# Performance work log

Hardware: AMD Instinct MI355X
Metric: run time of the kernel (lower is better)

## Reference

```python
import jax, jax.numpy as jnp
import numpy as np

NUM_GRAPHS = 100
NODES_PER_GRAPH = 500
EDGES_PER_GRAPH = 4000
HIDDEN = 128
RATIO = 0.5


def setup_inputs() -> dict:
    key = jax.random.key(0)
    k1, k2, k3, k4, k5 = jax.random.split(key, 5)
    N = NUM_GRAPHS * NODES_PER_GRAPH
    E = NUM_GRAPHS * EDGES_PER_GRAPH
    emb = jax.random.normal(k1, (N, HIDDEN), dtype=jnp.float32)
    # edges stay within their own graph's node range
    offs = (jnp.arange(NUM_GRAPHS, dtype=jnp.int32) * NODES_PER_GRAPH)[:, None]
    src = jax.random.randint(k2, (NUM_GRAPHS, EDGES_PER_GRAPH), 0, NODES_PER_GRAPH, dtype=jnp.int32) + offs
    dst = jax.random.randint(k3, (NUM_GRAPHS, EDGES_PER_GRAPH), 0, NODES_PER_GRAPH, dtype=jnp.int32) + offs
    edge_index = jnp.stack([src.reshape(-1), dst.reshape(-1)], axis=0)  # [2, E]
    node_batch = jnp.repeat(jnp.arange(NUM_GRAPHS, dtype=jnp.int32), NODES_PER_GRAPH)  # [N]
    s1 = 1.0 / np.sqrt(2 * HIDDEN)
    s2 = 1.0 / np.sqrt(4 * HIDDEN)
    W1 = jax.random.normal(k4, (2 * HIDDEN, 4 * HIDDEN), dtype=jnp.float32) * s1
    b1 = jnp.zeros((4 * HIDDEN,), dtype=jnp.float32)
    W2 = jax.random.normal(k5, (4 * HIDDEN, 1), dtype=jnp.float32) * s2
    b2 = jnp.zeros((1,), dtype=jnp.float32)
    return {"emb": emb, "edge_index": edge_index, "node_batch": node_batch,
            "W1": W1, "b1": b1, "W2": W2, "b2": b2}


def reference(emb, edge_index, node_batch, W1, b1, W2, b2):
    row, col = edge_index[0], edge_index[1]
    E = row.shape[0]
    N = emb.shape[0]

    # --- edge attention: gather endpoint embeddings, concat, 2-layer MLP ---
    edge_rep = jnp.concatenate([emb[row], emb[col]], axis=-1)       # [E, 2H]
    h = jax.nn.relu(edge_rep @ W1 + b1)                              # [E, 4H]
    edge_att = (h @ W2 + b2)[:, 0]                                   # [E]

    # --- per-graph top-k split (split_graph with ratio) ---
    edge_graph = node_batch[row]                                     # [E]
    order = jnp.lexsort((-edge_att, edge_graph))                     # sort by graph, desc score
    counts = jax.ops.segment_sum(jnp.ones(E, jnp.int32), edge_graph,
                                 num_segments=NUM_GRAPHS)            # edges per graph
    offsets = jnp.concatenate([jnp.zeros(1, jnp.int32),
                               jnp.cumsum(counts)[:-1].astype(jnp.int32)])
    g_sorted = edge_graph[order]
    rank = jnp.arange(E, dtype=jnp.int32) - offsets[g_sorted]        # rank within graph
    k_per_graph = jnp.ceil(RATIO * counts.astype(jnp.float32)).astype(jnp.int32)
    causal_sorted = rank < k_per_graph[g_sorted]
    causal_mask = jnp.zeros(E, dtype=bool).at[order].set(causal_sorted)

    causal_edge_weight = jnp.where(causal_mask, edge_att, 0.0)
    spu_edge_weight = jnp.where(causal_mask, 0.0, edge_att)

    # --- relabel: compact node ids for the causal subgraph ---
    cm = causal_mask.astype(jnp.int32)
    deg = jnp.zeros(N, jnp.int32).at[row].add(cm).at[col].add(cm)
    node_mask = deg > 0                                              # nodes kept in causal subgraph
    new_id = jnp.cumsum(node_mask.astype(jnp.int32)) - 1             # compacted ids
    new_row = jnp.where(causal_mask, new_id[row], -1)
    new_col = jnp.where(causal_mask, new_id[col], -1)
    causal_edge_index = jnp.stack([new_row, new_col], axis=0)        # [2, E], -1 = dropped
    causal_x = jnp.where(node_mask[:, None], emb, 0.0)               # masked node features

    return (edge_att, causal_edge_weight, spu_edge_weight,
            causal_mask, causal_edge_index, node_mask, causal_x)
```

## Files before the change

kernel.cpp:

```cpp
#include <hip/hip_runtime.h>
#include <hip/hip_bf16.h>

#define NG      100
#define NPG     500
#define EPG     4000
#define HID     128
#define NNODES  (NG*NPG)
#define NE      (NG*EPG)
#define KSEL    2000
#define NB_SCAN ((NNODES + 255) / 256)

#define MAXB    1024
#define NRC     8
#define RJT     8
#define DELTA   0.03125f

#define O_ATT   0
#define O_CEW   (NE)
#define O_SEW   (2*NE)
#define O_MASK  (3*NE)
#define O_CEI   (4*NE)
#define O_NMASK (6*NE)
#define O_CX    (6*NE + NNODES)

typedef __attribute__((ext_vector_type(8))) short  short8;
typedef __attribute__((ext_vector_type(8))) __bf16 bf16x8;
typedef __attribute__((ext_vector_type(4))) float  f32x4;

#define MFMA16(a,b,c) __builtin_amdgcn_mfma_f32_16x16x32_bf16( \
    __builtin_bit_cast(bf16x8,(a)), __builtin_bit_cast(bf16x8,(b)), (c), 0, 0, 0)

#define GLOAD_LDS16(g, l) __builtin_amdgcn_global_load_lds( \
    (const __attribute__((address_space(1))) unsigned int*)(g), \
    (__attribute__((address_space(3)))       unsigned int*)(l), 16, 0, 0)

__device__ __forceinline__ unsigned short tobf(float x) {
    __hip_bfloat16 hb = __float2bfloat16(x);
    return *(unsigned short*)&hb;
}

#define PREP_TOBF 6250
#define PREP_PACK 512
#define PREP_DEG  49
#define PREP_GRID (PREP_TOBF + PREP_PACK + PREP_DEG + 1)

__global__ __launch_bounds__(256)
void prep_kernel(const float* __restrict__ emb, const float* __restrict__ W1,
                 unsigned short* __restrict__ eb, unsigned short* __restrict__ ph,
                 float* __restrict__ deg, int* __restrict__ bcnt)
{
    const int blk = blockIdx.x;
    const int t   = threadIdx.x;
    if (blk < PREP_TOBF) {
        int i = blk * 256 + t;
        float4 v = ((const float4*)emb)[i];
        ushort4 h;
        h.x = tobf(v.x); h.y = tobf(v.y); h.z = tobf(v.z); h.w = tobf(v.w);
        ((ushort4*)eb)[i] = h;
    } else if (blk < PREP_TOBF + PREP_PACK) {
        int idx  = (blk - PREP_TOBF) * 256 + t;
        int i    = idx & 7;
        int lane = (idx >> 3) & 63;
        int g    = idx >> 9;
        int jsub = g & 3;
        int rem  = g >> 2;
        int jo   = rem & 7;
        int kc   = rem >> 3;
        int j = jo * 64 + jsub * 16 + (lane & 15);
        int k = kc * 32 + (lane >> 4) * 8 + i;
        ph[idx] = tobf(W1[k * 512 + j]);
    } else if (blk < PREP_TOBF + PREP_PACK + PREP_DEG) {
        int i4 = (blk - PREP_TOBF - PREP_PACK) * 256 + t;
        if (i4 < NNODES / 4) ((float4*)deg)[i4] = make_float4(0.f, 0.f, 0.f, 0.f);
    } else {
        if (t < NG) bcnt[t] = 0;
    }
}

__global__ __launch_bounds__(256)
void att5_kernel(const unsigned short* __restrict__ embb,
                 const unsigned short* __restrict__ w1p,
                 const int* __restrict__ ei,
                 const float* __restrict__ b1,
                 const float* __restrict__ W2,
                 const float* __restrict__ b2,
                 float* __restrict__ out)
{
    __shared__ __align__(16) unsigned short ldsB[16384];

    const int t    = threadIdx.x;
    const int w    = t >> 6;
    const int lane = t & 63;
    const int r16  = lane & 15;
    const int quad = lane >> 4;

    const int e_base = blockIdx.x * 256 + w * 64;
    const char* eb = (const char*)embb;

    f32x4 A[4][8];
#pragma unroll
    for (int mt = 0; mt < 4; ++mt) {
        int e = min(e_base + mt * 16 + r16, NE - 1);
        const char* sp = eb + (ei[e] << 8);
        const char* dp = eb + (ei[NE + e] << 8);
#pragma unroll
        for (int k4 = 0; k4 < 4; ++k4) {
            A[mt][k4]     = *(const f32x4*)(sp + k4 * 64 + quad * 16);
            A[mt][k4 + 4] = *(const f32x4*)(dp + k4 * 64 + quad * 16);
        }
    }

    float attP[4][4];
#pragma unroll
    for (int mt = 0; mt < 4; ++mt)
#pragma unroll
        for (int rg = 0; rg < 4; ++rg) attP[mt][rg] = 0.0f;

#define STAGE(s_, buf_)                                                      \
    {                                                                        \
        _Pragma("unroll")                                                    \
        for (int cc = 0; cc < 4; ++cc) {                                     \
            int c2   = w * 4 + cc;                                           \
            int kc   = c2 >> 1;                                              \
            int jsub = ((s_) & 1) * 2 + (c2 & 1);                            \
            int jo   = (s_) >> 1;                                            \
            int g    = (kc * 8 + jo) * 4 + jsub;                             \
            GLOAD_LDS16(w1p + g * 512 + lane * 8,                            \
                        ldsB + (buf_) * 8192 + c2 * 512);                    \
        }                                                                    \
    }

    STAGE(0, 0);
    __syncthreads();

    for (int s = 0; s < 16; ++s) {
        const int cur = s & 1;
        if (s < 15) STAGE(s + 1, cur ^ 1);

#pragma unroll
        for (int jsub2 = 0; jsub2 < 2; ++jsub2) {
            f32x4 acc[4];
#pragma unroll
            for (int mt = 0; mt < 4; ++mt) acc[mt] = f32x4{};

#pragma unroll
            for (int kc = 0; kc < 8; ++kc) {
                short8 B = *(const short8*)(ldsB + cur * 8192 +
                                            (kc * 2 + jsub2) * 512 + lane * 8);
#pragma unroll
                for (int mt = 0; mt < 4; ++mt)
                    acc[mt] = MFMA16(A[mt][kc], B, acc[mt]);
            }

            const int j = s * 32 + jsub2 * 16 + r16;
            const float b1v = b1[j], w2v = W2[j];
#pragma unroll
            for (int mt = 0; mt < 4; ++mt)
#pragma unroll
                for (int rg = 0; rg < 4; ++rg)
                    attP[mt][rg] += fmaxf(acc[mt][rg] + b1v, 0.0f) * w2v;
        }
        __syncthreads();
    }
#undef STAGE

#pragma unroll
    for (int mt = 0; mt < 4; ++mt)
#pragma unroll
        for (int rg = 0; rg < 4; ++rg) {
            float v = attP[mt][rg];
#pragma unroll
            for (int msk = 1; msk <= 8; msk <<= 1) v += __shfl_xor(v, msk, 64);
            attP[mt][rg] = v;
        }

    const float bias2 = b2[0];
    if (r16 < 4) {
#pragma unroll
        for (int mt = 0; mt < 4; ++mt) {
            const int row = quad * 4 + r16;
            const int e   = e_base + mt * 16 + row;
            if (e < NE) out[O_ATT + e] = attP[mt][r16] + bias2;
        }
    }
}

__device__ __forceinline__ unsigned enc_key(float f) {
    unsigned u = __float_as_uint(f);
    return (u & 0x80000000u) ? ~u : (u | 0x80000000u);
}
__device__ __forceinline__ float dec_key(unsigned k) {
    unsigned u = (k & 0x80000000u) ? (k ^ 0x80000000u) : ~k;
    return __uint_as_float(u);
}

__device__ __forceinline__ int wave_sum(int c) {
#pragma unroll
    for (int m = 1; m <= 32; m <<= 1) c += __shfl_xor(c, m, 64);
    return c;
}

__global__ __launch_bounds__(256)
void topk4_kernel(const int* __restrict__ ei, float* __restrict__ out,
                  float* __restrict__ deg, int* __restrict__ bcnt,
                  int* __restrict__ need, int* __restrict__ blist)
{
    __shared__ int cnt;

    const int g  = blockIdx.x;
    const int t  = threadIdx.x;
    const int e0 = g * EPG;
    const int cbase = t * 16;
    const bool act = (t < 250);

    unsigned kreg[16];
    if (act) {
#pragma unroll
        for (int q4 = 0; q4 < 4; ++q4) {
            float4 v = *(const float4*)&out[O_ATT + e0 + cbase + q4 * 4];
            kreg[q4 * 4 + 0] = enc_key(v.x);
            kreg[q4 * 4 + 1] = enc_key(v.y);
            kreg[q4 * 4 + 2] = enc_key(v.z);
            kreg[q4 * 4 + 3] = enc_key(v.w);
        }
    }

    unsigned lo = 0u, hi = 0xFFFFFFFFu;
    while (lo < hi) {
        unsigned mid = lo + ((hi - lo) >> 1) + 1u;
        if (t == 0) cnt = 0;
        __syncthreads();
        int c = 0;
        if (act) {
#pragma unroll
            for (int q = 0; q < 16; ++q) c += (kreg[q] >= mid) ? 1 : 0;
        }
        c = wave_sum(c);
        if ((t & 63) == 0 && c) atomicAdd(&cnt, c);
        __syncthreads();
        int f = cnt;
        if (f >= KSEL) lo = mid; else hi = mid - 1u;
        __syncthreads();
    }
    const unsigned K = lo;
    const float v = dec_key(K);
    const unsigned khi = enc_key(v + DELTA);
    const unsigned klo = enc_key(v - DELTA);

    if (t == 0) cnt = 0;
    __syncthreads();
    {
        int c = 0;
        if (act) {
#pragma unroll
            for (int q = 0; q < 16; ++q) c += (kreg[q] > khi) ? 1 : 0;
        }
        c = wave_sum(c);
        if ((t & 63) == 0 && c) atomicAdd(&cnt, c);
    }
    __syncthreads();
    if (t == 0) need[g] = KSEL - cnt;

    if (act) {
#pragma unroll
        for (int q = 0; q < 16; ++q) {
            unsigned kk = kreg[q];
            int ge = e0 + cbase + q;
            float a = dec_key(kk);
            if (kk > khi) {
                out[O_CEW + ge]  = a;
                out[O_SEW + ge]  = 0.0f;
                out[O_MASK + ge] = 1.0f;
                atomicAdd(&deg[ei[ge]], 1.0f);
                atomicAdd(&deg[ei[NE + ge]], 1.0f);
            } else if (kk < klo) {
                out[O_CEW + ge]  = 0.0f;
                out[O_SEW + ge]  = a;
                out[O_MASK + ge] = 0.0f;
            } else {
                int p = atomicAdd(&bcnt[g], 1);
                if (p < MAXB) blist[g * MAXB + p] = ge;
            }
        }
    }
}

#define TE_  128
#define PADX 132
#define PADW 68

__global__ __launch_bounds__(256)
void repair_kernel(const float* __restrict__ emb, const int* __restrict__ ei,
                   const float* __restrict__ W1, const float* __restrict__ b1,
                   const float* __restrict__ W2,
                   const int* __restrict__ bcnt, const int* __restrict__ blist,
                   float* __restrict__ attx8)
{
    const int blk = blockIdx.x;
    const int ch  = blk / (NG * RJT);
    const int rem = blk - ch * (NG * RJT);
    const int g   = rem >> 3;
    const int jt  = rem & 7;
    const int bc  = min(bcnt[g], MAXB);
    if (ch * 128 >= bc) return;
    const int live = min(bc - ch * 128, TE_);

    __shared__ __align__(16) float Xs[32 * PADX];
    __shared__ __align__(16) float Ws[32 * PADW];
    __shared__ int sidx[TE_], cidx[TE_];

    const int t = threadIdx.x;
    if (t < TE_) {
        int lid = ch * 128 + t;
        int lc  = min(lid, bc - 1);
        int e   = blist[g * MAXB + lc];
        sidx[t] = ei[e];
        cidx[t] = ei[NE + e];
    }
    __syncthreads();

    const int te = t & 15;
    const int tj = t >> 4;
    const bool alive = (te * 8 < live);

    float acc[8][4];
#pragma unroll
    for (int a = 0; a < 8; ++a)
#pragma unroll
        for (int b = 0; b < 4; ++b) acc[a][b] = 0.0f;

    for (int kt = 0; kt < 8; ++kt) {
        __syncthreads();
#pragma unroll
        for (int i = 0; i < 4; ++i) {
            int flat = i * 256 + t;
            int e  = flat >> 3;
            if (e < live) {
                int k4 = flat & 7;
                int k  = kt * 32 + k4 * 4;
                const float* src;
                if (k < HID) src = emb + (long)sidx[e] * HID + k;
                else         src = emb + (long)cidx[e] * HID + (k - HID);
                float4 v = *(const float4*)src;
                int kl = k4 * 4;
                Xs[(kl + 0) * PADX + e] = v.x;
                Xs[(kl + 1) * PADX + e] = v.y;
                Xs[(kl + 2) * PADX + e] = v.z;
                Xs[(kl + 3) * PADX + e] = v.w;
            }
        }
#pragma unroll
        for (int i = 0; i < 2; ++i) {
            int flat = i * 256 + t;
            int kl = flat >> 4;
            int j4 = flat & 15;
            float4 v = *(const float4*)&W1[(kt * 32 + kl) * 512 + jt * 64 + j4 * 4];
            *(float4*)&Ws[kl * PADW + j4 * 4] = v;
        }
        __syncthreads();

        if (alive) {
#pragma unroll 4
            for (int kl = 0; kl < 32; ++kl) {
                float4 xa = *(const float4*)&Xs[kl * PADX + te * 8];
                float4 xb = *(const float4*)&Xs[kl * PADX + te * 8 + 4];
                float4 wa = *(const float4*)&Ws[kl * PADW + tj * 4];
                float xv[8] = {xa.x, xa.y, xa.z, xa.w, xb.x, xb.y, xb.z, xb.w};
                float wv[4] = {wa.x, wa.y, wa.z, wa.w};
#pragma unroll
                for (int a = 0; a < 8; ++a)
#pragma unroll
                    for (int b = 0; b < 4; ++b)
                        acc[a][b] = fmaf(xv[a], wv[b], acc[a][b]);
            }
        }
    }

    __syncthreads();
    float* red = Xs;
    if (alive) {
        const int jb = jt * 64 + tj * 4;
        float4 b1a = *(const float4*)&b1[jb];
        float4 w2a = *(const float4*)&W2[jb];
        float bv[4] = {b1a.x, b1a.y, b1a.z, b1a.w};
        float wv[4] = {w2a.x, w2a.y, w2a.z, w2a.w};
#pragma unroll
        for (int a = 0; a < 8; ++a) {
            float s = 0.0f;
#pragma unroll
            for (int b = 0; b < 4; ++b)
                s = fmaf(fmaxf(acc[a][b] + bv[b], 0.0f), wv[b], s);
            red[tj * 136 + te * 8 + a] = s;
        }
    }
    __syncthreads();
    if (t < TE_ && t < live) {
        float s = 0.0f;
#pragma unroll
        for (int q = 0; q < 16; ++q) s += red[q * 136 + t];
        attx8[(g * MAXB + ch * 128 + t) * RJT + jt] = s;
    }
}

__global__ __launch_bounds__(256)
void select_kernel(const int* __restrict__ ei, const int* __restrict__ bcnt,
                   const int* __restrict__ need, const int* __restrict__ blist,
                   const float* __restrict__ attx8, const float* __restrict__ b2,
                   float* __restrict__ out, float* __restrict__ deg)
{
    __shared__ float sa[MAXB];
    __shared__ int   si[MAXB];
    const int g = blockIdx.x;
    const int t = threadIdx.x;
    const int b = min(bcnt[g], MAXB);
    const int n = need[g];
    const float bias2 = b2[0];

    for (int i = t; i < b; i += 256) {
        float s = bias2;
#pragma unroll
        for (int jt = 0; jt < RJT; ++jt)
            s += attx8[(g * MAXB + i) * RJT + jt];
        sa[i] = s;
        si[i] = blist[g * MAXB + i];
    }
    __syncthreads();

    for (int i = t; i < b; i += 256) {
        float ai = sa[i];
        int   ii = si[i];
        int rank = 0;
        for (int j = 0; j < b; ++j)
            rank += (sa[j] > ai || (sa[j] == ai && si[j] < ii)) ? 1 : 0;
        bool flag = rank < n;
        out[O_CEW + ii]  = flag ? ai : 0.0f;
        out[O_SEW + ii]  = flag ? 0.0f : ai;
        out[O_MASK + ii] = flag ? 1.0f : 0.0f;
        if (flag) {
            atomicAdd(&deg[ei[ii]], 1.0f);
            atomicAdd(&deg[ei[NE + ii]], 1.0f);
        }
    }
}

__global__ __launch_bounds__(256)
void scanA(const float* __restrict__ deg, int* __restrict__ partials)
{
    __shared__ int s[256];
    int t = threadIdx.x;
    int n = blockIdx.x * 256 + t;
    int m = (n < NNODES && deg[n] > 0.5f) ? 1 : 0;
    s[t] = m;
    __syncthreads();
    for (int off = 128; off > 0; off >>= 1) {
        if (t < off) s[t] += s[t + off];
        __syncthreads();
    }
    if (t == 0) partials[blockIdx.x] = s[0];
}

__global__ __launch_bounds__(256)
void scanC(float* __restrict__ deg_nm, const int* __restrict__ partials,
           int* __restrict__ newid)
{
    __shared__ int s[256];
    __shared__ int p[256];
    int t = threadIdx.x;
    int b = blockIdx.x;
    int n = b * 256 + t;

    p[t] = (t < NB_SCAN && t < b) ? partials[t] : 0;
    __syncthreads();
    for (int off = 128; off > 0; off >>= 1) {
        if (t < off) p[t] += p[t + off];
        __syncthreads();
    }
    const int ex_b = p[0];
    __syncthreads();

    int m = (n < NNODES && deg_nm[n] > 0.5f) ? 1 : 0;
    s[t] = m;
    __syncthreads();
    for (int off = 1; off < 256; off <<= 1) {
        int x = (t >= off) ? s[t - off] : 0;
        __syncthreads();
        s[t] += x;
        __syncthreads();
    }
    if (n < NNODES) {
        newid[n]  = ex_b + s[t] - 1;
        deg_nm[n] = m ? 1.0f : 0.0f;
    }
}

#define FIN_EDGE 1563
#define FIN_GRID (FIN_EDGE + 6250)

__global__ __launch_bounds__(256)
void final_kernel(const float* __restrict__ emb, const int* __restrict__ ei,
                  const int* __restrict__ newid, const float* __restrict__ nm,
                  float* __restrict__ out)
{
    const int blk = blockIdx.x;
    const int t   = threadIdx.x;
    if (blk < FIN_EDGE) {
        int e = blk * 256 + t;
        if (e >= NE) return;
        bool flag = out[O_MASK + e] > 0.5f;
        int row = ei[e];
        int col = ei[NE + e];
        out[O_CEI + e]      = flag ? (float)newid[row] : -1.0f;
        out[O_CEI + NE + e] = flag ? (float)newid[col] : -1.0f;
    } else {
        int i4 = (blk - FIN_EDGE) * 256 + t;
        if (i4 >= NNODES * HID / 4) return;
        int n = i4 >> 5;
        float4 v = ((const float4*)emb)[i4];
        if (!(nm[n] > 0.5f)) v = make_float4(0.0f, 0.0f, 0.0f, 0.0f);
        ((float4*)(out + O_CX))[i4] = v;
    }
}

extern "C" void kernel_launch(void* const* d_in, const int* in_sizes, int n_in,
                              void* d_out, int out_size, void* d_ws, size_t ws_size,
                              hipStream_t stream)
{
    const float* emb = (const float*)d_in[0];
    const int*   ei  = (const int*)d_in[1];
    const float* W1  = (const float*)d_in[3];
    const float* b1  = (const float*)d_in[4];
    const float* W2  = (const float*)d_in[5];
    const float* b2  = (const float*)d_in[6];
    float* out = (float*)d_out;

    char* wsb = (char*)d_ws;
    int*   newid    = (int*)wsb;
    int*   partials = (int*)(wsb + 200704);
    int*   bcnt     = (int*)(wsb + 201728);
    int*   need     = (int*)(wsb + 202752);
    int*   blist    = (int*)(wsb + 203776);
    float* attx8    = (float*)(wsb + 203776 + NG*MAXB*4);
    unsigned short* embb = (unsigned short*)(wsb + 203776 + NG*MAXB*4 + NG*MAXB*RJT*4);
    unsigned short* w1p  = embb + NNODES * HID;
    float* deg = out + O_NMASK;

    prep_kernel<<<PREP_GRID, 256, 0, stream>>>(emb, W1, embb, w1p, deg, bcnt);
    att5_kernel<<<(NE + 255) / 256, 256, 0, stream>>>(embb, w1p, ei, b1, W2, b2, out);
    topk4_kernel<<<NG, 256, 0, stream>>>(ei, out, deg, bcnt, need, blist);
    repair_kernel<<<NG * NRC * RJT, 256, 0, stream>>>(emb, ei, W1, b1, W2,
                                                      bcnt, blist, attx8);
    select_kernel<<<NG, 256, 0, stream>>>(ei, bcnt, need, blist, attx8, b2, out, deg);
    scanA<<<NB_SCAN, 256, 0, stream>>>(deg, partials);
    scanC<<<NB_SCAN, 256, 0, stream>>>(deg, partials, newid);
    final_kernel<<<FIN_GRID, 256, 0, stream>>>(emb, ei, newid, deg, out);
}
```

Before: 361.1 us.

## Fuse select, scan and final kernels into one cooperative persistent kernel

Replaces the four tail kernels (select, scanA, scanC, final) with a single cooperative kernel of 1024 blocks. Each former stage becomes a grid-stride loop, and grid.sync() separates the stages. The goal is to remove three kernel launch gaps and their inter-kernel drains. In exchange, the select stage uses only 100 of the 1024 blocks, the large final copy is limited to a fixed grid, and grid-wide barriers add their own overhead.

Result: slower. 637.7 us (+76.6%).

```diff
diff --git a/kernel.cpp b/kernel.cpp
--- a/kernel.cpp
+++ b/kernel.cpp
@@ -1,5 +1,8 @@
 #include <hip/hip_runtime.h>
 #include <hip/hip_bf16.h>
+#include <hip/hip_cooperative_groups.h>
+
+namespace cg = cooperative_groups;
 
 #define NG      100
 #define NPG     500
@@ -402,122 +405,124 @@
     }
 }
 
+#define TAIL_GRID 1024
+
 __global__ __launch_bounds__(256)
-void select_kernel(const int* __restrict__ ei, const int* __restrict__ bcnt,
-                   const int* __restrict__ need, const int* __restrict__ blist,
-                   const float* __restrict__ attx8, const float* __restrict__ b2,
-                   float* __restrict__ out, float* __restrict__ deg)
+void tail_kernel(const int* __restrict__ ei, const int* __restrict__ bcnt,
+                 const int* __restrict__ need, const int* __restrict__ blist,
+                 const float* __restrict__ attx8, const float* __restrict__ b2,
+                 float* __restrict__ out, float* __restrict__ deg,
+                 int* __restrict__ partials, int* __restrict__ newid,
+                 const float* __restrict__ emb)
 {
+    cg::grid_group grid = cg::this_grid();
+    const int t = threadIdx.x;
+
     __shared__ float sa[MAXB];
     __shared__ int   si[MAXB];
-    const int g = blockIdx.x;
-    const int t = threadIdx.x;
-    const int b = min(bcnt[g], MAXB);
-    const int n = need[g];
-    const float bias2 = b2[0];
-
-    for (int i = t; i < b; i += 256) {
-        float s = bias2;
-#pragma unroll
-        for (int jt = 0; jt < RJT; ++jt)
-            s += attx8[(g * MAXB + i) * RJT + jt];
-        sa[i] = s;
-        si[i] = blist[g * MAXB + i];
-    }
-    __syncthreads();
-
-    for (int i = t; i < b; i += 256) {
-        float ai = sa[i];
-        int   ii = si[i];
-        int rank = 0;
-        for (int j = 0; j < b; ++j)
-            rank += (sa[j] > ai || (sa[j] == ai && si[j] < ii)) ? 1 : 0;
-        bool flag = rank < n;
-        out[O_CEW + ii]  = flag ? ai : 0.0f;
-        out[O_SEW + ii]  = flag ? 0.0f : ai;
-        out[O_MASK + ii] = flag ? 1.0f : 0.0f;
-        if (flag) {
-            atomicAdd(&deg[ei[ii]], 1.0f);
-            atomicAdd(&deg[ei[NE + ii]], 1.0f);
-        }
-    }
-}
-
-__global__ __launch_bounds__(256)
-void scanA(const float* __restrict__ deg, int* __restrict__ partials)
-{
-    __shared__ int s[256];
-    int t = threadIdx.x;
-    int n = blockIdx.x * 256 + t;
-    int m = (n < NNODES && deg[n] > 0.5f) ? 1 : 0;
-    s[t] = m;
-    __syncthreads();
-    for (int off = 128; off > 0; off >>= 1) {
-        if (t < off) s[t] += s[t + off];
-        __syncthreads();
-    }
-    if (t == 0) partials[blockIdx.x] = s[0];
-}
-
-__global__ __launch_bounds__(256)
-void scanC(float* __restrict__ deg_nm, const int* __restrict__ partials,
-           int* __restrict__ newid)
-{
-    __shared__ int s[256];
-    __shared__ int p[256];
-    int t = threadIdx.x;
-    int b = blockIdx.x;
-    int n = b * 256 + t;
-
-    p[t] = (t < NB_SCAN && t < b) ? partials[t] : 0;
-    __syncthreads();
-    for (int off = 128; off > 0; off >>= 1) {
-        if (t < off) p[t] += p[t + off];
-        __syncthreads();
-    }
-    const int ex_b = p[0];
-    __syncthreads();
-
-    int m = (n < NNODES && deg_nm[n] > 0.5f) ? 1 : 0;
-    s[t] = m;
-    __syncthreads();
-    for (int off = 1; off < 256; off <<= 1) {
-        int x = (t >= off) ? s[t - off] : 0;
-        __syncthreads();
-        s[t] += x;
-        __syncthreads();
-    }
-    if (n < NNODES) {
-        newid[n]  = ex_b + s[t] - 1;
-        deg_nm[n] = m ? 1.0f : 0.0f;
-    }
-}
+
+    for (int g = blockIdx.x; g < NG; g += gridDim.x) {
+        const int b = min(bcnt[g], MAXB);
+        const int n = need[g];
+        const float bias2 = b2[0];
+
+        for (int i = t; i < b; i += 256) {
+            float s = bias2;
+#pragma unroll
+            for (int jt = 0; jt < RJT; ++jt)
+                s += attx8[(g * MAXB + i) * RJT + jt];
+            sa[i] = s;
+            si[i] = blist[g * MAXB + i];
+        }
+        __syncthreads();
+
+        for (int i = t; i < b; i += 256) {
+            float ai = sa[i];
+            int   ii = si[i];
+            int rank = 0;
+            for (int j = 0; j < b; ++j)
+                rank += (sa[j] > ai || (sa[j] == ai && si[j] < ii)) ? 1 : 0;
+            bool flag = rank < n;
+            out[O_CEW + ii]  = flag ? ai : 0.0f;
+            out[O_SEW + ii]  = flag ? 0.0f : ai;
+            out[O_MASK + ii] = flag ? 1.0f : 0.0f;
+            if (flag) {
+                atomicAdd(&deg[ei[ii]], 1.0f);
+                atomicAdd(&deg[ei[NE + ii]], 1.0f);
+            }
+        }
+        __syncthreads();
+    }
+
+    grid.sync();
+
+    int* s4 = si;
+    for (int vb = blockIdx.x; vb < NB_SCAN; vb += gridDim.x) {
+        int n = vb * 256 + t;
+        int m = (n < NNODES && deg[n] > 0.5f) ? 1 : 0;
+        s4[t] = m;
+        __syncthreads();
+        for (int off = 128; off > 0; off >>= 1) {
+            if (t < off) s4[t] += s4[t + off];
+            __syncthreads();
+        }
+        if (t == 0) partials[vb] = s4[0];
+        __syncthreads();
+    }
+
+    grid.sync();
+
+    int* p4 = (int*)sa;
+    for (int vb = blockIdx.x; vb < NB_SCAN; vb += gridDim.x) {
+        p4[t] = (t < NB_SCAN && t < vb) ? partials[t] : 0;
+        __syncthreads();
+        for (int off = 128; off > 0; off >>= 1) {
+            if (t < off) p4[t] += p4[t + off];
+            __syncthreads();
+        }
+        const int ex_b = p4[0];
+        __syncthreads();
+
+        int n = vb * 256 + t;
+        int m = (n < NNODES && deg[n] > 0.5f) ? 1 : 0;
+        s4[t] = m;
+        __syncthreads();
+        for (int off = 1; off < 256; off <<= 1) {
+            int x = (t >= off) ? s4[t - off] : 0;
+            __syncthreads();
+            s4[t] += x;
+            __syncthreads();
+        }
+        if (n < NNODES) {
+            newid[n] = ex_b + s4[t] - 1;
+            deg[n]   = m ? 1.0f : 0.0f;
+        }
+        __syncthreads();
+    }
+
+    grid.sync();
 
 #define FIN_EDGE 1563
 #define FIN_GRID (FIN_EDGE + 6250)
-
-__global__ __launch_bounds__(256)
-void final_kernel(const float* __restrict__ emb, const int* __restrict__ ei,
-                  const int* __restrict__ newid, const float* __restrict__ nm,
-                  float* __restrict__ out)
-{
-    const int blk = blockIdx.x;
-    const int t   = threadIdx.x;
-    if (blk < FIN_EDGE) {
-        int e = blk * 256 + t;
-        if (e >= NE) return;
-        bool flag = out[O_MASK + e] > 0.5f;
-        int row = ei[e];
-        int col = ei[NE + e];
-        out[O_CEI + e]      = flag ? (float)newid[row] : -1.0f;
-        out[O_CEI + NE + e] = flag ? (float)newid[col] : -1.0f;
-    } else {
-        int i4 = (blk - FIN_EDGE) * 256 + t;
-        if (i4 >= NNODES * HID / 4) return;
-        int n = i4 >> 5;
-        float4 v = ((const float4*)emb)[i4];
-        if (!(nm[n] > 0.5f)) v = make_float4(0.0f, 0.0f, 0.0f, 0.0f);
-        ((float4*)(out + O_CX))[i4] = v;
+    for (int vb = blockIdx.x; vb < FIN_GRID; vb += gridDim.x) {
+        if (vb < FIN_EDGE) {
+            int e = vb * 256 + t;
+            if (e < NE) {
+                bool flag = out[O_MASK + e] > 0.5f;
+                int row = ei[e];
+                int col = ei[NE + e];
+                out[O_CEI + e]      = flag ? (float)newid[row] : -1.0f;
+                out[O_CEI + NE + e] = flag ? (float)newid[col] : -1.0f;
+            }
+        } else {
+            int i4 = (vb - FIN_EDGE) * 256 + t;
+            if (i4 < NNODES * HID / 4) {
+                int n = i4 >> 5;
+                float4 v = ((const float4*)emb)[i4];
+                if (!(deg[n] > 0.5f)) v = make_float4(0.0f, 0.0f, 0.0f, 0.0f);
+                ((float4*)(out + O_CX))[i4] = v;
+            }
+        }
     }
 }
 
@@ -549,8 +554,10 @@
     topk4_kernel<<<NG, 256, 0, stream>>>(ei, out, deg, bcnt, need, blist);
     repair_kernel<<<NG * NRC * RJT, 256, 0, stream>>>(emb, ei, W1, b1, W2,
                                                       bcnt, blist, attx8);
-    select_kernel<<<NG, 256, 0, stream>>>(ei, bcnt, need, blist, attx8, b2, out, deg);
-    scanA<<<NB_SCAN, 256, 0, stream>>>(deg, partials);
-    scanC<<<NB_SCAN, 256, 0, stream>>>(deg, partials, newid);
-    final_kernel<<<FIN_GRID, 256, 0, stream>>>(emb, ei, newid, deg, out);
-}
+
+    void* args[] = {(void*)&ei, (void*)&bcnt, (void*)&need, (void*)&blist,
+                    (void*)&attx8, (void*)&b2, (void*)&out, (void*)&deg,
+                    (void*)&partials, (void*)&newid, (void*)&emb};
+    hipLaunchCooperativeKernel((void*)tail_kernel, dim3(TAIL_GRID), dim3(256),
+                               args, 0, stream);
+}
```
